# Optimization experiments

Hardware: AMD Instinct MI355X
Metric: run time of the kernel (lower is better)

The kernel has to match this reference:

```python
import jax, jax.numpy as jnp
import numpy as np

B, N = 2, 65536
V, VSUB, J, R = 6890, 689, 24, 64
THRESH = 0.12


def trilinear(grid, coords):
    # grid: [C, D, H, W]; coords: [..., 3] in [-1, 1] (x->W, y->H, z->D)
    C, D, H, W = grid.shape
    cs = jnp.clip(coords.reshape(-1, 3), -1.0, 1.0)
    x = (cs[:, 0] + 1.0) * 0.5 * (W - 1)
    y = (cs[:, 1] + 1.0) * 0.5 * (H - 1)
    z = (cs[:, 2] + 1.0) * 0.5 * (D - 1)
    x0 = jnp.floor(x).astype(jnp.int32); x1 = jnp.minimum(x0 + 1, W - 1)
    y0 = jnp.floor(y).astype(jnp.int32); y1 = jnp.minimum(y0 + 1, H - 1)
    z0 = jnp.floor(z).astype(jnp.int32); z1 = jnp.minimum(z0 + 1, D - 1)
    fx = x - x0; fy = y - y0; fz = z - z0
    g = lambda zi, yi, xi: grid[:, zi, yi, xi]  # [C, M]
    out = (g(z0, y0, x0) * ((1 - fz) * (1 - fy) * (1 - fx))
         + g(z0, y0, x1) * ((1 - fz) * (1 - fy) * fx)
         + g(z0, y1, x0) * ((1 - fz) * fy * (1 - fx))
         + g(z0, y1, x1) * ((1 - fz) * fy * fx)
         + g(z1, y0, x0) * (fz * (1 - fy) * (1 - fx))
         + g(z1, y0, x1) * (fz * (1 - fy) * fx)
         + g(z1, y1, x0) * (fz * fy * (1 - fx))
         + g(z1, y1, x1) * (fz * fy * fx))
    return out.T.reshape(coords.shape[:-1] + (C,))


def setup_inputs() -> dict:
    key = jax.random.key(0)
    ks = jax.random.split(key, 8)
    pts_in = jax.random.normal(ks[0], (B, N, 3), jnp.float32) * 0.4
    vs_template = jax.random.normal(ks[1], (1, VSUB, 3), jnp.float32) * 0.4
    shape_offset = jax.random.normal(ks[2], (1, V, 3), jnp.float32) * 0.01
    init_idx = jax.random.randint(ks[3], (N, 3), 0, V, jnp.int32)
    bar = jax.random.uniform(ks[4], (N, 3), jnp.float32) + 1e-3
    init_bar = bar / jnp.sum(bar, -1, keepdims=True)
    lbs_voxel = jax.nn.softmax(jax.random.normal(ks[5], (J, R, R, R), jnp.float32), axis=0)
    tfs = jnp.tile(jnp.eye(4, dtype=jnp.float32), (B, J, 1, 1)) \
        + 0.05 * jax.random.normal(ks[6], (B, J, 4, 4), jnp.float32)
    grid_scale = jnp.full((3,), 1.5, jnp.float32)
    grid_offset = jnp.zeros((3,), jnp.float32)
    return dict(pts_in=pts_in, vs_template=vs_template, shape_offset=shape_offset,
                init_idx=init_idx, init_bar=init_bar, lbs_voxel=lbs_voxel,
                tfs=tfs, grid_scale=grid_scale, grid_offset=grid_offset)


def reference(pts_in, vs_template, shape_offset, init_idx, init_bar, lbs_voxel, tfs, grid_scale, grid_offset):
    # --- KNN (K=1) against subsampled template vertices ---
    v = vs_template[0]  # [VSUB, 3]
    d2 = (jnp.sum(pts_in * pts_in, -1, keepdims=True)
          + jnp.sum(v * v, -1)[None, None, :]
          - 2.0 * jnp.einsum('bnd,vd->bnv', pts_in, v))  # [B,N,VSUB]
    dist_sq = jnp.min(d2, axis=-1)  # [B,N]
    mask = (dist_sq < THRESH ** 2)[..., None]  # [B,N,1]
    # --- barycentric interpolation of per-vertex shape offsets ---
    tri = shape_offset[0][init_idx]               # [N,3,3]
    off = jnp.sum(init_bar[..., None] * tri, -2)  # [N,3]
    pts = pts_in + off[None]
    # --- query LBS weights from explicit voxel grid (fast-SNARF) ---
    pts_norm = (pts - grid_offset) * grid_scale
    w = trilinear(lbs_voxel, pts_norm)  # [B,N,J]
    w = w / jnp.clip(jnp.sum(w, -1, keepdims=True), 1e-6, None)
    # --- forward skinning ---
    w_tf = jnp.einsum('bnj,bjkl->bnkl', w, tfs)  # [B,N,4,4]
    pts_h = jnp.concatenate([pts, jnp.ones_like(pts[..., :1])], -1)  # [B,N,4]
    pts_posed = jnp.einsum('bnkl,bnl->bnk', w_tf, pts_h)[..., :3]
    pts_cano_all = pts_posed.reshape(B, N, 1, 3)
    return pts_cano_all, mask, w_tf
```

## Files before the change

kernel.cpp:

```cpp
#include <hip/hip_runtime.h>
#include <math.h>

#define NB    2
#define NPTS  65536
#define NVSUB 689
#define NJ    24
#define GR    64
#define GRV   (GR*GR*GR)
#define THRESH2 0.0144f

#define O_PTS  0
#define O_MASK (NB*NPTS*3)
#define O_WTF  (O_MASK + NB*NPTS)

__global__ __launch_bounds__(256) void transpose_grid(const float* __restrict__ g,
                                                      float* __restrict__ gt) {
    int vox = blockIdx.x * 256 + threadIdx.x;
    float v[NJ];
#pragma unroll
    for (int c = 0; c < NJ; ++c) v[c] = g[c * GRV + vox];
    float4* dst = (float4*)(gt + (size_t)vox * NJ);
#pragma unroll
    for (int c4 = 0; c4 < 6; ++c4)
        dst[c4] = make_float4(v[4*c4+0], v[4*c4+1], v[4*c4+2], v[4*c4+3]);
}

template <bool TRANSPOSED>
__device__ inline void process_point(int b, int n, float qx, float qy, float qz,
                                     float dist2,
                                     const float* __restrict__ grid,
                                     const float* __restrict__ s_tfs,
                                     float gsx, float gsy, float gsz,
                                     float gox, float goy, float goz,
                                     float* __restrict__ out) {
    float cx = fminf(fmaxf((qx - gox) * gsx, -1.f), 1.f);
    float cy = fminf(fmaxf((qy - goy) * gsy, -1.f), 1.f);
    float cz = fminf(fmaxf((qz - goz) * gsz, -1.f), 1.f);
    float x = (cx + 1.f) * 0.5f * (GR - 1);
    float y = (cy + 1.f) * 0.5f * (GR - 1);
    float z = (cz + 1.f) * 0.5f * (GR - 1);
    int x0 = (int)floorf(x), y0 = (int)floorf(y), z0 = (int)floorf(z);
    int x1 = min(x0 + 1, GR - 1), y1 = min(y0 + 1, GR - 1), z1 = min(z0 + 1, GR - 1);
    float fx = x - (float)x0, fy = y - (float)y0, fz = z - (float)z0;
    float wx[2] = {1.f - fx, fx}, wy[2] = {1.f - fy, fy}, wz[2] = {1.f - fz, fz};

    float w[NJ];
#pragma unroll
    for (int c = 0; c < NJ; ++c) w[c] = 0.f;

#pragma unroll
    for (int ci = 0; ci < 8; ++ci) {
        int xi = (ci & 1) ? x1 : x0;
        int yi = (ci & 2) ? y1 : y0;
        int zi = (ci & 4) ? z1 : z0;
        float wt = wx[ci & 1] * wy[(ci >> 1) & 1] * wz[(ci >> 2) & 1];
        int vox = (zi * GR + yi) * GR + xi;
        if (TRANSPOSED) {
            const float4* g4 = (const float4*)(grid + (size_t)vox * NJ);
#pragma unroll
            for (int c4 = 0; c4 < 6; ++c4) {
                float4 gv = g4[c4];
                w[4*c4+0] = fmaf(wt, gv.x, w[4*c4+0]);
                w[4*c4+1] = fmaf(wt, gv.y, w[4*c4+1]);
                w[4*c4+2] = fmaf(wt, gv.z, w[4*c4+2]);
                w[4*c4+3] = fmaf(wt, gv.w, w[4*c4+3]);
            }
        } else {
#pragma unroll
            for (int c = 0; c < NJ; ++c)
                w[c] = fmaf(wt, grid[c * GRV + vox], w[c]);
        }
    }
    float s = 0.f;
#pragma unroll
    for (int c = 0; c < NJ; ++c) s += w[c];
    float inv = 1.f / fmaxf(s, 1e-6f);

    float acc[16];
#pragma unroll
    for (int k = 0; k < 16; ++k) acc[k] = 0.f;
    const float* tb = s_tfs + b * NJ * 16;
#pragma unroll
    for (int j = 0; j < NJ; ++j) {
        float wj = w[j] * inv;
#pragma unroll
        for (int k = 0; k < 16; ++k) acc[k] = fmaf(wj, tb[j * 16 + k], acc[k]);
    }

    float px = acc[0] * qx + acc[1] * qy + acc[2]  * qz + acc[3];
    float py = acc[4] * qx + acc[5] * qy + acc[6]  * qz + acc[7];
    float pz = acc[8] * qx + acc[9] * qy + acc[10] * qz + acc[11];

    size_t bn = (size_t)b * NPTS + n;
    out[O_PTS + bn * 3 + 0] = px;
    out[O_PTS + bn * 3 + 1] = py;
    out[O_PTS + bn * 3 + 2] = pz;
    out[O_MASK + bn] = (dist2 < THRESH2) ? 1.f : 0.f;
    float4* wt4 = (float4*)(out + O_WTF + bn * 16);
    wt4[0] = make_float4(acc[0],  acc[1],  acc[2],  acc[3]);
    wt4[1] = make_float4(acc[4],  acc[5],  acc[6],  acc[7]);
    wt4[2] = make_float4(acc[8],  acc[9],  acc[10], acc[11]);
    wt4[3] = make_float4(acc[12], acc[13], acc[14], acc[15]);
}

template <bool TRANSPOSED>
__global__ __launch_bounds__(256) void snarf_main(
    const float* __restrict__ pts_in,
    const float* __restrict__ vs,
    const float* __restrict__ shape_off,
    const int*   __restrict__ init_idx,
    const float* __restrict__ init_bar,
    const float* __restrict__ grid,
    const float* __restrict__ tfs,
    const float* __restrict__ gscale,
    const float* __restrict__ goff,
    float* __restrict__ out) {
    __shared__ float4 s_vs[NVSUB];
    __shared__ float  s_tfs[NB * NJ * 16];
    const int tid = threadIdx.x;
    for (int i = tid; i < NVSUB; i += 256) {
        float x = vs[i * 3 + 0], y = vs[i * 3 + 1], z = vs[i * 3 + 2];
        s_vs[i] = make_float4(x, y, z, x * x + y * y + z * z);
    }
    for (int i = tid; i < NB * NJ * 16; i += 256) s_tfs[i] = tfs[i];
    __syncthreads();

    const int n = blockIdx.x * 256 + tid;

    float p0x = pts_in[n * 3 + 0], p0y = pts_in[n * 3 + 1], p0z = pts_in[n * 3 + 2];
    float p1x = pts_in[(NPTS + n) * 3 + 0], p1y = pts_in[(NPTS + n) * 3 + 1],
          p1z = pts_in[(NPTS + n) * 3 + 2];
    float pp0 = p0x * p0x + p0y * p0y + p0z * p0z;
    float pp1 = p1x * p1x + p1y * p1y + p1z * p1z;

    float m0 = 3.4e38f, m1 = 3.4e38f;
#pragma unroll 4
    for (int v = 0; v < NVSUB; ++v) {
        float4 t = s_vs[v];
        float d0 = p0x * t.x + p0y * t.y + p0z * t.z;
        float d1 = p1x * t.x + p1y * t.y + p1z * t.z;
        m0 = fminf(m0, fmaf(-2.f, d0, t.w));
        m1 = fminf(m1, fmaf(-2.f, d1, t.w));
    }
    float dist2_0 = m0 + pp0;
    float dist2_1 = m1 + pp1;

    int i0 = init_idx[n * 3 + 0] * 3;
    int i1 = init_idx[n * 3 + 1] * 3;
    int i2 = init_idx[n * 3 + 2] * 3;
    float b0 = init_bar[n * 3 + 0], b1 = init_bar[n * 3 + 1], b2 = init_bar[n * 3 + 2];
    float ox = b0 * shape_off[i0 + 0] + b1 * shape_off[i1 + 0] + b2 * shape_off[i2 + 0];
    float oy = b0 * shape_off[i0 + 1] + b1 * shape_off[i1 + 1] + b2 * shape_off[i2 + 1];
    float oz = b0 * shape_off[i0 + 2] + b1 * shape_off[i1 + 2] + b2 * shape_off[i2 + 2];

    float gsx = gscale[0], gsy = gscale[1], gsz = gscale[2];
    float gox = goff[0],   goy = goff[1],   goz = goff[2];

    process_point<TRANSPOSED>(0, n, p0x + ox, p0y + oy, p0z + oz, dist2_0,
                              grid, s_tfs, gsx, gsy, gsz, gox, goy, goz, out);
    process_point<TRANSPOSED>(1, n, p1x + ox, p1y + oy, p1z + oz, dist2_1,
                              grid, s_tfs, gsx, gsy, gsz, gox, goy, goz, out);
}

extern "C" void kernel_launch(void* const* d_in, const int* in_sizes, int n_in,
                              void* d_out, int out_size, void* d_ws, size_t ws_size,
                              hipStream_t stream) {
    const float* pts_in    = (const float*)d_in[0];
    const float* vs        = (const float*)d_in[1];
    const float* shape_off = (const float*)d_in[2];
    const int*   init_idx  = (const int*)d_in[3];
    const float* init_bar  = (const float*)d_in[4];
    const float* lbs       = (const float*)d_in[5];
    const float* tfs       = (const float*)d_in[6];
    const float* gs        = (const float*)d_in[7];
    const float* go        = (const float*)d_in[8];
    float* out = (float*)d_out;

    const size_t needed = (size_t)GRV * NJ * sizeof(float);
    if (ws_size >= needed) {
        float* gT = (float*)d_ws;
        transpose_grid<<<GRV / 256, 256, 0, stream>>>(lbs, gT);
        snarf_main<true><<<NPTS / 256, 256, 0, stream>>>(
            pts_in, vs, shape_off, init_idx, init_bar, gT, tfs, gs, go, out);
    } else {
        snarf_main<false><<<NPTS / 256, 256, 0, stream>>>(
            pts_in, vs, shape_off, init_idx, init_bar, lbs, tfs, gs, go, out);
    }
}
```

Measured before the change: 151.6 us.

## Split KNN search across four waves per point group and parallelize batch processing

Each block now handles 64 points, and its four waves each scan a quarter of the template vertices. The partial minima are reduced through shared memory, then two waves each process one batch element's trilinear interpolation and skinning. Before, each thread did the full 689-vertex scan serially for 256 points per block, launching only 256 blocks. The new layout gives four times as many blocks and divides the scan work, at the cost of an extra barrier, idle waves during the skinning phase, and each block reloading the vertex table. It also adds a launch-bounds occupancy hint and a fast reciprocal.

```diff
diff --git a/kernel.cpp b/kernel.cpp
--- a/kernel.cpp
+++ b/kernel.cpp
@@ -74,7 +74,7 @@
     float s = 0.f;
 #pragma unroll
     for (int c = 0; c < NJ; ++c) s += w[c];
-    float inv = 1.f / fmaxf(s, 1e-6f);
+    float inv = __builtin_amdgcn_rcpf(fmaxf(s, 1e-6f));
 
     float acc[16];
 #pragma unroll
@@ -104,7 +104,7 @@
 }
 
 template <bool TRANSPOSED>
-__global__ __launch_bounds__(256) void snarf_main(
+__global__ __launch_bounds__(256, 4) void snarf_main(
     const float* __restrict__ pts_in,
     const float* __restrict__ vs,
     const float* __restrict__ shape_off,
@@ -117,7 +117,12 @@
     float* __restrict__ out) {
     __shared__ float4 s_vs[NVSUB];
     __shared__ float  s_tfs[NB * NJ * 16];
+    __shared__ float  s_m[NB][4][64];
     const int tid = threadIdx.x;
+    const int q  = tid >> 6;
+    const int nl = tid & 63;
+    const int n = blockIdx.x * 64 + nl;
+
     for (int i = tid; i < NVSUB; i += 256) {
         float x = vs[i * 3 + 0], y = vs[i * 3 + 1], z = vs[i * 3 + 2];
         s_vs[i] = make_float4(x, y, z, x * x + y * y + z * z);
@@ -125,41 +130,54 @@
     for (int i = tid; i < NB * NJ * 16; i += 256) s_tfs[i] = tfs[i];
     __syncthreads();
 
-    const int n = blockIdx.x * 256 + tid;
-
-    float p0x = pts_in[n * 3 + 0], p0y = pts_in[n * 3 + 1], p0z = pts_in[n * 3 + 2];
-    float p1x = pts_in[(NPTS + n) * 3 + 0], p1y = pts_in[(NPTS + n) * 3 + 1],
-          p1z = pts_in[(NPTS + n) * 3 + 2];
-    float pp0 = p0x * p0x + p0y * p0y + p0z * p0z;
-    float pp1 = p1x * p1x + p1y * p1y + p1z * p1z;
-
-    float m0 = 3.4e38f, m1 = 3.4e38f;
-#pragma unroll 4
-    for (int v = 0; v < NVSUB; ++v) {
-        float4 t = s_vs[v];
-        float d0 = p0x * t.x + p0y * t.y + p0z * t.z;
-        float d1 = p1x * t.x + p1y * t.y + p1z * t.z;
-        m0 = fminf(m0, fmaf(-2.f, d0, t.w));
-        m1 = fminf(m1, fmaf(-2.f, d1, t.w));
-    }
-    float dist2_0 = m0 + pp0;
-    float dist2_1 = m1 + pp1;
-
-    int i0 = init_idx[n * 3 + 0] * 3;
-    int i1 = init_idx[n * 3 + 1] * 3;
-    int i2 = init_idx[n * 3 + 2] * 3;
-    float b0 = init_bar[n * 3 + 0], b1 = init_bar[n * 3 + 1], b2 = init_bar[n * 3 + 2];
-    float ox = b0 * shape_off[i0 + 0] + b1 * shape_off[i1 + 0] + b2 * shape_off[i2 + 0];
-    float oy = b0 * shape_off[i0 + 1] + b1 * shape_off[i1 + 1] + b2 * shape_off[i2 + 1];
-    float oz = b0 * shape_off[i0 + 2] + b1 * shape_off[i1 + 2] + b2 * shape_off[i2 + 2];
-
-    float gsx = gscale[0], gsy = gscale[1], gsz = gscale[2];
-    float gox = goff[0],   goy = goff[1],   goz = goff[2];
-
-    process_point<TRANSPOSED>(0, n, p0x + ox, p0y + oy, p0z + oz, dist2_0,
-                              grid, s_tfs, gsx, gsy, gsz, gox, goy, goz, out);
-    process_point<TRANSPOSED>(1, n, p1x + ox, p1y + oy, p1z + oz, dist2_1,
-                              grid, s_tfs, gsx, gsy, gsz, gox, goy, goz, out);
+    const float p0x = pts_in[n * 3 + 0], p0y = pts_in[n * 3 + 1], p0z = pts_in[n * 3 + 2];
+    const float p1x = pts_in[(NPTS + n) * 3 + 0], p1y = pts_in[(NPTS + n) * 3 + 1],
+                p1z = pts_in[(NPTS + n) * 3 + 2];
+
+    const int vbeg = q * 173;
+    const int vend = min(vbeg + 173, NVSUB);
+    float m0a = 3.4e38f, m0b = 3.4e38f, m1a = 3.4e38f, m1b = 3.4e38f;
+    int v = vbeg;
+    for (; v + 2 <= vend; v += 2) {
+        float4 ta = s_vs[v];
+        float4 tb = s_vs[v + 1];
+        m0a = fminf(m0a, fmaf(-2.f, p0x * ta.x + p0y * ta.y + p0z * ta.z, ta.w));
+        m1a = fminf(m1a, fmaf(-2.f, p1x * ta.x + p1y * ta.y + p1z * ta.z, ta.w));
+        m0b = fminf(m0b, fmaf(-2.f, p0x * tb.x + p0y * tb.y + p0z * tb.z, tb.w));
+        m1b = fminf(m1b, fmaf(-2.f, p1x * tb.x + p1y * tb.y + p1z * tb.z, tb.w));
+    }
+    if (v < vend) {
+        float4 ta = s_vs[v];
+        m0a = fminf(m0a, fmaf(-2.f, p0x * ta.x + p0y * ta.y + p0z * ta.z, ta.w));
+        m1a = fminf(m1a, fmaf(-2.f, p1x * ta.x + p1y * ta.y + p1z * ta.z, ta.w));
+    }
+    s_m[0][q][nl] = fminf(m0a, m0b);
+    s_m[1][q][nl] = fminf(m1a, m1b);
+    __syncthreads();
+
+    if (q < 2) {
+        float mm = fminf(fminf(s_m[q][0][nl], s_m[q][1][nl]),
+                         fminf(s_m[q][2][nl], s_m[q][3][nl]));
+        int i0 = init_idx[n * 3 + 0] * 3;
+        int i1 = init_idx[n * 3 + 1] * 3;
+        int i2 = init_idx[n * 3 + 2] * 3;
+        float b0 = init_bar[n * 3 + 0], b1 = init_bar[n * 3 + 1], b2 = init_bar[n * 3 + 2];
+        float ox = b0 * shape_off[i0 + 0] + b1 * shape_off[i1 + 0] + b2 * shape_off[i2 + 0];
+        float oy = b0 * shape_off[i0 + 1] + b1 * shape_off[i1 + 1] + b2 * shape_off[i2 + 1];
+        float oz = b0 * shape_off[i0 + 2] + b1 * shape_off[i1 + 2] + b2 * shape_off[i2 + 2];
+
+        float px = (q == 0) ? p0x : p1x;
+        float py = (q == 0) ? p0y : p1y;
+        float pz = (q == 0) ? p0z : p1z;
+        float pp = px * px + py * py + pz * pz;
+        float dist2 = mm + pp;
+
+        float gsx = gscale[0], gsy = gscale[1], gsz = gscale[2];
+        float gox = goff[0],   goy = goff[1],   goz = goff[2];
+
+        process_point<TRANSPOSED>(q, n, px + ox, py + oy, pz + oz, dist2,
+                                  grid, s_tfs, gsx, gsy, gsz, gox, goy, goz, out);
+    }
 }
 
 extern "C" void kernel_launch(void* const* d_in, const int* in_sizes, int n_in,
@@ -180,10 +198,10 @@
     if (ws_size >= needed) {
         float* gT = (float*)d_ws;
         transpose_grid<<<GRV / 256, 256, 0, stream>>>(lbs, gT);
-        snarf_main<true><<<NPTS / 256, 256, 0, stream>>>(
+        snarf_main<true><<<NPTS / 64, 256, 0, stream>>>(
             pts_in, vs, shape_off, init_idx, init_bar, gT, tfs, gs, go, out);
     } else {
-        snarf_main<false><<<NPTS / 256, 256, 0, stream>>>(
+        snarf_main<false><<<NPTS / 64, 256, 0, stream>>>(
             pts_in, vs, shape_off, init_idx, init_bar, lbs, tfs, gs, go, out);
     }
 }
```

New measurement: 132.2 us. 12.8% less time.

## Split KNN and per-joint skinning work across four waves per point group

Applied to the files above, without the earlier changes.

The main kernel now handles 64 points per 256-thread block. Each of four waves scans a quarter of the template vertices for the nearest-neighbour search, and waves are then paired per batch so each computes half the joints' trilinear weights and skinning partials. The partials are combined through shared memory. Template vertex preprocessing moves into the prep kernel, and transforms are read from global memory through uniform (readfirstlane) addresses instead of shared memory. This spreads the work over four times as many blocks to raise occupancy and parallelism, at the cost of redundant offset and trilinear setup, extra barriers and a shared-memory reduction.

```diff
diff --git a/kernel.cpp b/kernel.cpp
--- a/kernel.cpp
+++ b/kernel.cpp
@@ -13,29 +13,95 @@
 #define O_MASK (NB*NPTS*3)
 #define O_WTF  (O_MASK + NB*NPTS)
 
-__global__ __launch_bounds__(256) void transpose_grid(const float* __restrict__ g,
-                                                      float* __restrict__ gt) {
-    int vox = blockIdx.x * 256 + threadIdx.x;
-    float v[NJ];
-#pragma unroll
-    for (int c = 0; c < NJ; ++c) v[c] = g[c * GRV + vox];
-    float4* dst = (float4*)(gt + (size_t)vox * NJ);
-#pragma unroll
-    for (int c4 = 0; c4 < 6; ++c4)
-        dst[c4] = make_float4(v[4*c4+0], v[4*c4+1], v[4*c4+2], v[4*c4+3]);
-}
-
-template <bool TRANSPOSED>
-__device__ inline void process_point(int b, int n, float qx, float qy, float qz,
-                                     float dist2,
-                                     const float* __restrict__ grid,
-                                     const float* __restrict__ s_tfs,
-                                     float gsx, float gsy, float gsz,
-                                     float gox, float goy, float goz,
-                                     float* __restrict__ out) {
-    float cx = fminf(fmaxf((qx - gox) * gsx, -1.f), 1.f);
-    float cy = fminf(fmaxf((qy - goy) * gsy, -1.f), 1.f);
-    float cz = fminf(fmaxf((qz - goz) * gsz, -1.f), 1.f);
+#define WS_VS4_OFF (GRV * NJ)
+
+__global__ __launch_bounds__(256) void prep_kernel(const float* __restrict__ g,
+                                                   const float* __restrict__ vs,
+                                                   float* __restrict__ ws) {
+    if (blockIdx.x < GRV / 256) {
+        int vox = blockIdx.x * 256 + threadIdx.x;
+        float v[NJ];
+#pragma unroll
+        for (int c = 0; c < NJ; ++c) v[c] = g[c * GRV + vox];
+        float4* dst = (float4*)(ws + (size_t)vox * NJ);
+#pragma unroll
+        for (int c4 = 0; c4 < 6; ++c4)
+            dst[c4] = make_float4(v[4*c4+0], v[4*c4+1], v[4*c4+2], v[4*c4+3]);
+    } else {
+        float4* vs4 = (float4*)(ws + WS_VS4_OFF);
+        for (int i = threadIdx.x; i < NVSUB; i += 256) {
+            float x = vs[i * 3 + 0], y = vs[i * 3 + 1], z = vs[i * 3 + 2];
+            vs4[i] = make_float4(x, y, z, x * x + y * y + z * z);
+        }
+    }
+}
+
+__global__ __launch_bounds__(256, 4) void snarf_main(
+    const float* __restrict__ pts_in,
+    const float* __restrict__ shape_off,
+    const int*   __restrict__ init_idx,
+    const float* __restrict__ init_bar,
+    const float* __restrict__ ws,
+    const float* __restrict__ tfs,
+    const float* __restrict__ gscale,
+    const float* __restrict__ goff,
+    float* __restrict__ out) {
+    __shared__ float s_m[NB][4][64];
+    __shared__ float s_part[NB][64][20];
+
+    const int tid  = threadIdx.x;
+    const int q    = tid >> 6;
+    const int nl   = tid & 63;
+    const int b    = q & 1;
+    const int half = q >> 1;
+    const int n    = blockIdx.x * 64 + nl;
+
+    const float4* vs4 = (const float4*)(ws + WS_VS4_OFF);
+    const float*  gT  = ws;
+
+    const float p0x = pts_in[n * 3 + 0], p0y = pts_in[n * 3 + 1], p0z = pts_in[n * 3 + 2];
+    const float p1x = pts_in[(NPTS + n) * 3 + 0], p1y = pts_in[(NPTS + n) * 3 + 1],
+                p1z = pts_in[(NPTS + n) * 3 + 2];
+
+    const int vbeg = q * 172 + (q != 0);
+    const int vend = (q + 1) * 172 + 1;
+    float m0a = 3.4e38f, m0b = 3.4e38f, m1a = 3.4e38f, m1b = 3.4e38f;
+    int v = vbeg;
+    for (; v + 4 <= vend; v += 4) {
+        float4 t0 = vs4[v], t1 = vs4[v + 1], t2 = vs4[v + 2], t3 = vs4[v + 3];
+        m0a = fminf(m0a, fmaf(-2.f, p0x * t0.x + p0y * t0.y + p0z * t0.z, t0.w));
+        m1a = fminf(m1a, fmaf(-2.f, p1x * t0.x + p1y * t0.y + p1z * t0.z, t0.w));
+        m0b = fminf(m0b, fmaf(-2.f, p0x * t1.x + p0y * t1.y + p0z * t1.z, t1.w));
+        m1b = fminf(m1b, fmaf(-2.f, p1x * t1.x + p1y * t1.y + p1z * t1.z, t1.w));
+        m0a = fminf(m0a, fmaf(-2.f, p0x * t2.x + p0y * t2.y + p0z * t2.z, t2.w));
+        m1a = fminf(m1a, fmaf(-2.f, p1x * t2.x + p1y * t2.y + p1z * t2.z, t2.w));
+        m0b = fminf(m0b, fmaf(-2.f, p0x * t3.x + p0y * t3.y + p0z * t3.z, t3.w));
+        m1b = fminf(m1b, fmaf(-2.f, p1x * t3.x + p1y * t3.y + p1z * t3.z, t3.w));
+    }
+    for (; v < vend; ++v) {
+        float4 t0 = vs4[v];
+        m0a = fminf(m0a, fmaf(-2.f, p0x * t0.x + p0y * t0.y + p0z * t0.z, t0.w));
+        m1a = fminf(m1a, fmaf(-2.f, p1x * t0.x + p1y * t0.y + p1z * t0.z, t0.w));
+    }
+    s_m[0][q][nl] = fminf(m0a, m0b);
+    s_m[1][q][nl] = fminf(m1a, m1b);
+    __syncthreads();
+
+    int i0 = init_idx[n * 3 + 0] * 3;
+    int i1 = init_idx[n * 3 + 1] * 3;
+    int i2 = init_idx[n * 3 + 2] * 3;
+    float b0 = init_bar[n * 3 + 0], b1 = init_bar[n * 3 + 1], b2 = init_bar[n * 3 + 2];
+    float ox = b0 * shape_off[i0 + 0] + b1 * shape_off[i1 + 0] + b2 * shape_off[i2 + 0];
+    float oy = b0 * shape_off[i0 + 1] + b1 * shape_off[i1 + 1] + b2 * shape_off[i2 + 1];
+    float oz = b0 * shape_off[i0 + 2] + b1 * shape_off[i1 + 2] + b2 * shape_off[i2 + 2];
+
+    const float qx = (b ? p1x : p0x) + ox;
+    const float qy = (b ? p1y : p0y) + oy;
+    const float qz = (b ? p1z : p0z) + oz;
+
+    float cx = fminf(fmaxf((qx - goff[0]) * gscale[0], -1.f), 1.f);
+    float cy = fminf(fmaxf((qy - goff[1]) * gscale[1], -1.f), 1.f);
+    float cz = fminf(fmaxf((qz - goff[2]) * gscale[2], -1.f), 1.f);
     float x = (cx + 1.f) * 0.5f * (GR - 1);
     float y = (cy + 1.f) * 0.5f * (GR - 1);
     float z = (cz + 1.f) * 0.5f * (GR - 1);
@@ -44,9 +110,10 @@
     float fx = x - (float)x0, fy = y - (float)y0, fz = z - (float)z0;
     float wx[2] = {1.f - fx, fx}, wy[2] = {1.f - fy, fy}, wz[2] = {1.f - fz, fz};
 
-    float w[NJ];
-#pragma unroll
-    for (int c = 0; c < NJ; ++c) w[c] = 0.f;
+    const int jbeg = half * 12;
+    float w[12];
+#pragma unroll
+    for (int c = 0; c < 12; ++c) w[c] = 0.f;
 
 #pragma unroll
     for (int ci = 0; ci < 8; ++ci) {
@@ -55,111 +122,130 @@
         int zi = (ci & 4) ? z1 : z0;
         float wt = wx[ci & 1] * wy[(ci >> 1) & 1] * wz[(ci >> 2) & 1];
         int vox = (zi * GR + yi) * GR + xi;
-        if (TRANSPOSED) {
-            const float4* g4 = (const float4*)(grid + (size_t)vox * NJ);
-#pragma unroll
-            for (int c4 = 0; c4 < 6; ++c4) {
-                float4 gv = g4[c4];
-                w[4*c4+0] = fmaf(wt, gv.x, w[4*c4+0]);
-                w[4*c4+1] = fmaf(wt, gv.y, w[4*c4+1]);
-                w[4*c4+2] = fmaf(wt, gv.z, w[4*c4+2]);
-                w[4*c4+3] = fmaf(wt, gv.w, w[4*c4+3]);
-            }
-        } else {
-#pragma unroll
-            for (int c = 0; c < NJ; ++c)
-                w[c] = fmaf(wt, grid[c * GRV + vox], w[c]);
-        }
-    }
-    float s = 0.f;
-#pragma unroll
-    for (int c = 0; c < NJ; ++c) s += w[c];
-    float inv = 1.f / fmaxf(s, 1e-6f);
-
+        const float4* g4 = (const float4*)(gT + (size_t)vox * NJ + jbeg);
+        float4 g0 = g4[0], g1 = g4[1], g2 = g4[2];
+        w[0]  = fmaf(wt, g0.x, w[0]);  w[1]  = fmaf(wt, g0.y, w[1]);
+        w[2]  = fmaf(wt, g0.z, w[2]);  w[3]  = fmaf(wt, g0.w, w[3]);
+        w[4]  = fmaf(wt, g1.x, w[4]);  w[5]  = fmaf(wt, g1.y, w[5]);
+        w[6]  = fmaf(wt, g1.z, w[6]);  w[7]  = fmaf(wt, g1.w, w[7]);
+        w[8]  = fmaf(wt, g2.x, w[8]);  w[9]  = fmaf(wt, g2.y, w[9]);
+        w[10] = fmaf(wt, g2.z, w[10]); w[11] = fmaf(wt, g2.w, w[11]);
+    }
+    float wsum = 0.f;
+#pragma unroll
+    for (int c = 0; c < 12; ++c) wsum += w[c];
+
+    const int bu = __builtin_amdgcn_readfirstlane(b);
+    const int jbu = __builtin_amdgcn_readfirstlane(jbeg);
+    const float* tb = tfs + (size_t)(bu * NJ + jbu) * 16;
     float acc[16];
 #pragma unroll
     for (int k = 0; k < 16; ++k) acc[k] = 0.f;
-    const float* tb = s_tfs + b * NJ * 16;
-#pragma unroll
-    for (int j = 0; j < NJ; ++j) {
-        float wj = w[j] * inv;
-#pragma unroll
-        for (int k = 0; k < 16; ++k) acc[k] = fmaf(wj, tb[j * 16 + k], acc[k]);
-    }
-
-    float px = acc[0] * qx + acc[1] * qy + acc[2]  * qz + acc[3];
-    float py = acc[4] * qx + acc[5] * qy + acc[6]  * qz + acc[7];
-    float pz = acc[8] * qx + acc[9] * qy + acc[10] * qz + acc[11];
-
-    size_t bn = (size_t)b * NPTS + n;
-    out[O_PTS + bn * 3 + 0] = px;
-    out[O_PTS + bn * 3 + 1] = py;
-    out[O_PTS + bn * 3 + 2] = pz;
-    out[O_MASK + bn] = (dist2 < THRESH2) ? 1.f : 0.f;
-    float4* wt4 = (float4*)(out + O_WTF + bn * 16);
-    wt4[0] = make_float4(acc[0],  acc[1],  acc[2],  acc[3]);
-    wt4[1] = make_float4(acc[4],  acc[5],  acc[6],  acc[7]);
-    wt4[2] = make_float4(acc[8],  acc[9],  acc[10], acc[11]);
-    wt4[3] = make_float4(acc[12], acc[13], acc[14], acc[15]);
-}
-
-template <bool TRANSPOSED>
-__global__ __launch_bounds__(256) void snarf_main(
-    const float* __restrict__ pts_in,
-    const float* __restrict__ vs,
-    const float* __restrict__ shape_off,
-    const int*   __restrict__ init_idx,
-    const float* __restrict__ init_bar,
-    const float* __restrict__ grid,
-    const float* __restrict__ tfs,
-    const float* __restrict__ gscale,
-    const float* __restrict__ goff,
-    float* __restrict__ out) {
-    __shared__ float4 s_vs[NVSUB];
-    __shared__ float  s_tfs[NB * NJ * 16];
-    const int tid = threadIdx.x;
-    for (int i = tid; i < NVSUB; i += 256) {
-        float x = vs[i * 3 + 0], y = vs[i * 3 + 1], z = vs[i * 3 + 2];
-        s_vs[i] = make_float4(x, y, z, x * x + y * y + z * z);
-    }
-    for (int i = tid; i < NB * NJ * 16; i += 256) s_tfs[i] = tfs[i];
+#pragma unroll
+    for (int jj = 0; jj < 12; ++jj) {
+        float wj = w[jj];
+#pragma unroll
+        for (int k = 0; k < 16; ++k) acc[k] = fmaf(wj, tb[jj * 16 + k], acc[k]);
+    }
+
+    if (half == 1) {
+        float* sp = &s_part[b][nl][0];
+        ((float4*)sp)[0] = make_float4(acc[0],  acc[1],  acc[2],  acc[3]);
+        ((float4*)sp)[1] = make_float4(acc[4],  acc[5],  acc[6],  acc[7]);
+        ((float4*)sp)[2] = make_float4(acc[8],  acc[9],  acc[10], acc[11]);
+        ((float4*)sp)[3] = make_float4(acc[12], acc[13], acc[14], acc[15]);
+        sp[16] = wsum;
+    }
     __syncthreads();
 
-    const int n = blockIdx.x * 256 + tid;
-
-    float p0x = pts_in[n * 3 + 0], p0y = pts_in[n * 3 + 1], p0z = pts_in[n * 3 + 2];
-    float p1x = pts_in[(NPTS + n) * 3 + 0], p1y = pts_in[(NPTS + n) * 3 + 1],
-          p1z = pts_in[(NPTS + n) * 3 + 2];
-    float pp0 = p0x * p0x + p0y * p0y + p0z * p0z;
-    float pp1 = p1x * p1x + p1y * p1y + p1z * p1z;
-
-    float m0 = 3.4e38f, m1 = 3.4e38f;
-#pragma unroll 4
-    for (int v = 0; v < NVSUB; ++v) {
-        float4 t = s_vs[v];
-        float d0 = p0x * t.x + p0y * t.y + p0z * t.z;
-        float d1 = p1x * t.x + p1y * t.y + p1z * t.z;
-        m0 = fminf(m0, fmaf(-2.f, d0, t.w));
-        m1 = fminf(m1, fmaf(-2.f, d1, t.w));
-    }
-    float dist2_0 = m0 + pp0;
-    float dist2_1 = m1 + pp1;
-
-    int i0 = init_idx[n * 3 + 0] * 3;
-    int i1 = init_idx[n * 3 + 1] * 3;
-    int i2 = init_idx[n * 3 + 2] * 3;
-    float b0 = init_bar[n * 3 + 0], b1 = init_bar[n * 3 + 1], b2 = init_bar[n * 3 + 2];
-    float ox = b0 * shape_off[i0 + 0] + b1 * shape_off[i1 + 0] + b2 * shape_off[i2 + 0];
-    float oy = b0 * shape_off[i0 + 1] + b1 * shape_off[i1 + 1] + b2 * shape_off[i2 + 1];
-    float oz = b0 * shape_off[i0 + 2] + b1 * shape_off[i1 + 2] + b2 * shape_off[i2 + 2];
-
-    float gsx = gscale[0], gsy = gscale[1], gsz = gscale[2];
-    float gox = goff[0],   goy = goff[1],   goz = goff[2];
-
-    process_point<TRANSPOSED>(0, n, p0x + ox, p0y + oy, p0z + oz, dist2_0,
-                              grid, s_tfs, gsx, gsy, gsz, gox, goy, goz, out);
-    process_point<TRANSPOSED>(1, n, p1x + ox, p1y + oy, p1z + oz, dist2_1,
-                              grid, s_tfs, gsx, gsy, gsz, gox, goy, goz, out);
+    if (half == 0) {
+        const float* sp = &s_part[b][nl][0];
+        float4 q0 = ((const float4*)sp)[0], q1 = ((const float4*)sp)[1];
+        float4 q2 = ((const float4*)sp)[2], q3 = ((const float4*)sp)[3];
+        acc[0] += q0.x;  acc[1] += q0.y;  acc[2] += q0.z;  acc[3] += q0.w;
+        acc[4] += q1.x;  acc[5] += q1.y;  acc[6] += q1.z;  acc[7] += q1.w;
+        acc[8] += q2.x;  acc[9] += q2.y;  acc[10] += q2.z; acc[11] += q2.w;
+        acc[12] += q3.x; acc[13] += q3.y; acc[14] += q3.z; acc[15] += q3.w;
+        wsum += sp[16];
+        float inv = __builtin_amdgcn_rcpf(fmaxf(wsum, 1e-6f));
+#pragma unroll
+        for (int k = 0; k < 16; ++k) acc[k] *= inv;
+
+        float px = acc[0] * qx + acc[1] * qy + acc[2]  * qz + acc[3];
+        float py = acc[4] * qx + acc[5] * qy + acc[6]  * qz + acc[7];
+        float pz = acc[8] * qx + acc[9] * qy + acc[10] * qz + acc[11];
+
+        float mm = fminf(fminf(s_m[b][0][nl], s_m[b][1][nl]),
+                         fminf(s_m[b][2][nl], s_m[b][3][nl]));
+        float pbx = b ? p1x : p0x, pby = b ? p1y : p0y, pbz = b ? p1z : p0z;
+        float dist2 = mm + pbx * pbx + pby * pby + pbz * pbz;
+
+        size_t bn = (size_t)b * NPTS + n;
+        out[O_PTS + bn * 3 + 0] = px;
+        out[O_PTS + bn * 3 + 1] = py;
+        out[O_PTS + bn * 3 + 2] = pz;
+        out[O_MASK + bn] = (dist2 < THRESH2) ? 1.f : 0.f;
+        float4* wt4 = (float4*)(out + O_WTF + bn * 16);
+        wt4[0] = make_float4(acc[0],  acc[1],  acc[2],  acc[3]);
+        wt4[1] = make_float4(acc[4],  acc[5],  acc[6],  acc[7]);
+        wt4[2] = make_float4(acc[8],  acc[9],  acc[10], acc[11]);
+        wt4[3] = make_float4(acc[12], acc[13], acc[14], acc[15]);
+    }
+}
+
+__global__ __launch_bounds__(256) void snarf_fallback(
+    const float* __restrict__ pts_in, const float* __restrict__ vs,
+    const float* __restrict__ shape_off, const int* __restrict__ init_idx,
+    const float* __restrict__ init_bar, const float* __restrict__ grid,
+    const float* __restrict__ tfs, const float* __restrict__ gscale,
+    const float* __restrict__ goff, float* __restrict__ out) {
+    const int n = blockIdx.x * 256 + threadIdx.x;
+    for (int b = 0; b < NB; ++b) {
+        float px = pts_in[((size_t)b * NPTS + n) * 3 + 0];
+        float py = pts_in[((size_t)b * NPTS + n) * 3 + 1];
+        float pz = pts_in[((size_t)b * NPTS + n) * 3 + 2];
+        float mm = 3.4e38f;
+        for (int v = 0; v < NVSUB; ++v) {
+            float dx = px - vs[v * 3 + 0], dy = py - vs[v * 3 + 1], dz = pz - vs[v * 3 + 2];
+            mm = fminf(mm, dx * dx + dy * dy + dz * dz);
+        }
+        int i0 = init_idx[n * 3 + 0] * 3, i1 = init_idx[n * 3 + 1] * 3, i2 = init_idx[n * 3 + 2] * 3;
+        float b0 = init_bar[n * 3 + 0], b1 = init_bar[n * 3 + 1], b2 = init_bar[n * 3 + 2];
+        float qx = px + b0 * shape_off[i0 + 0] + b1 * shape_off[i1 + 0] + b2 * shape_off[i2 + 0];
+        float qy = py + b0 * shape_off[i0 + 1] + b1 * shape_off[i1 + 1] + b2 * shape_off[i2 + 1];
+        float qz = pz + b0 * shape_off[i0 + 2] + b1 * shape_off[i1 + 2] + b2 * shape_off[i2 + 2];
+        float cx = fminf(fmaxf((qx - goff[0]) * gscale[0], -1.f), 1.f);
+        float cy = fminf(fmaxf((qy - goff[1]) * gscale[1], -1.f), 1.f);
+        float cz = fminf(fmaxf((qz - goff[2]) * gscale[2], -1.f), 1.f);
+        float x = (cx + 1.f) * 0.5f * (GR - 1), y = (cy + 1.f) * 0.5f * (GR - 1), z = (cz + 1.f) * 0.5f * (GR - 1);
+        int x0 = (int)floorf(x), y0 = (int)floorf(y), z0 = (int)floorf(z);
+        int x1 = min(x0 + 1, GR - 1), y1 = min(y0 + 1, GR - 1), z1 = min(z0 + 1, GR - 1);
+        float fx = x - x0, fy = y - y0, fz = z - z0;
+        float wxa[2] = {1.f - fx, fx}, wya[2] = {1.f - fy, fy}, wza[2] = {1.f - fz, fz};
+        float w[NJ];
+        for (int c = 0; c < NJ; ++c) w[c] = 0.f;
+        for (int ci = 0; ci < 8; ++ci) {
+            int xi = (ci & 1) ? x1 : x0, yi = (ci & 2) ? y1 : y0, zi = (ci & 4) ? z1 : z0;
+            float wt = wxa[ci & 1] * wya[(ci >> 1) & 1] * wza[(ci >> 2) & 1];
+            int vox = (zi * GR + yi) * GR + xi;
+            for (int c = 0; c < NJ; ++c) w[c] = fmaf(wt, grid[c * GRV + vox], w[c]);
+        }
+        float s = 0.f;
+        for (int c = 0; c < NJ; ++c) s += w[c];
+        float inv = 1.f / fmaxf(s, 1e-6f);
+        float acc[16];
+        for (int k = 0; k < 16; ++k) acc[k] = 0.f;
+        for (int j = 0; j < NJ; ++j) {
+            float wj = w[j] * inv;
+            for (int k = 0; k < 16; ++k) acc[k] = fmaf(wj, tfs[(b * NJ + j) * 16 + k], acc[k]);
+        }
+        size_t bn = (size_t)b * NPTS + n;
+        out[O_PTS + bn * 3 + 0] = acc[0] * qx + acc[1] * qy + acc[2] * qz + acc[3];
+        out[O_PTS + bn * 3 + 1] = acc[4] * qx + acc[5] * qy + acc[6] * qz + acc[7];
+        out[O_PTS + bn * 3 + 2] = acc[8] * qx + acc[9] * qy + acc[10] * qz + acc[11];
+        out[O_MASK + bn] = (mm < THRESH2) ? 1.f : 0.f;
+        for (int k = 0; k < 16; ++k) out[O_WTF + bn * 16 + k] = acc[k];
+    }
 }
 
 extern "C" void kernel_launch(void* const* d_in, const int* in_sizes, int n_in,
@@ -176,14 +262,14 @@
     const float* go        = (const float*)d_in[8];
     float* out = (float*)d_out;
 
-    const size_t needed = (size_t)GRV * NJ * sizeof(float);
+    const size_t needed = ((size_t)GRV * NJ + NVSUB * 4) * sizeof(float);
     if (ws_size >= needed) {
-        float* gT = (float*)d_ws;
-        transpose_grid<<<GRV / 256, 256, 0, stream>>>(lbs, gT);
-        snarf_main<true><<<NPTS / 256, 256, 0, stream>>>(
-            pts_in, vs, shape_off, init_idx, init_bar, gT, tfs, gs, go, out);
+        float* wsf = (float*)d_ws;
+        prep_kernel<<<GRV / 256 + 1, 256, 0, stream>>>(lbs, vs, wsf);
+        snarf_main<<<NPTS / 64, 256, 0, stream>>>(
+            pts_in, shape_off, init_idx, init_bar, wsf, tfs, gs, go, out);
     } else {
-        snarf_main<false><<<NPTS / 256, 256, 0, stream>>>(
+        snarf_fallback<<<NPTS / 256, 256, 0, stream>>>(
             pts_in, vs, shape_off, init_idx, init_bar, lbs, tfs, gs, go, out);
     }
 }
```

Result: faster. 146.2 us (-3.6%).
